# Optimization experiments

Hardware: AMD Instinct MI355X
Metric: run time of the kernel (lower is better)

## Reference

```python
import jax, jax.numpy as jnp
import numpy as np

B, T, I, H = 128, 512, 256, 512


def setup_inputs() -> dict:
    key = jax.random.key(0)
    ks = jax.random.split(key, 13)
    s_in = 1.0 / np.sqrt(I)
    s_h = 1.0 / np.sqrt(H)
    return {
        "x": jax.random.normal(ks[0], (B, T, I), jnp.float32),
        "h0": jnp.zeros((B, H), jnp.float32),
        "w_z": jax.random.normal(ks[1], (H, I), jnp.float32) * s_in,
        "w_r": jax.random.normal(ks[2], (H, I), jnp.float32) * s_in,
        "w_h": jax.random.normal(ks[3], (H, I), jnp.float32) * s_in,
        "r_z": jax.random.normal(ks[4], (H, H), jnp.float32) * s_h,
        "r_r": jax.random.normal(ks[5], (H, H), jnp.float32) * s_h,
        "r_h": jax.random.normal(ks[6], (H, H), jnp.float32) * s_h,
        "w_bz": jax.random.normal(ks[7], (H,), jnp.float32) * 0.1,
        "w_br": jax.random.normal(ks[8], (H,), jnp.float32) * 0.1,
        "w_bh": jax.random.normal(ks[9], (H,), jnp.float32) * 0.1,
        "r_bz": jax.random.normal(ks[10], (H,), jnp.float32) * 0.1,
        "r_br": jax.random.normal(ks[11], (H,), jnp.float32) * 0.1,
        "r_bh": jax.random.normal(ks[12], (H,), jnp.float32) * 0.1,
    }


def reference(x, h0, w_z, w_r, w_h, r_z, r_r, r_h,
              w_bz, w_br, w_bh, r_bz, r_br, r_bh):
    # ONNX GRU, linear_before_reset=0, no clip, activations = (sigmoid, tanh).
    # Precompute input-side projections across the whole sequence (same math
    # as per-step matmuls, done once as big GEMMs). Shapes: [B,T,H].
    xz = jnp.einsum('bti,hi->bth', x, w_z) + (w_bz + r_bz)
    xr = jnp.einsum('bti,hi->bth', x, w_r) + (w_br + r_br)
    xh = jnp.einsum('bti,hi->bth', x, w_h) + (w_bh + r_bh)

    # scan over time: carry h [B,H]
    def step(h, xs):
        xz_t, xr_t, xh_t = xs
        z = jax.nn.sigmoid(xz_t + h @ r_z.T)
        r = jax.nn.sigmoid(xr_t + h @ r_r.T)
        hh = jnp.tanh(xh_t + (r * h) @ r_h.T)
        h_new = (1.0 - z) * hh + z * h
        return h_new, h_new

    xs = (jnp.swapaxes(xz, 0, 1), jnp.swapaxes(xr, 0, 1), jnp.swapaxes(xh, 0, 1))
    h_last, seq = jax.lax.scan(step, h0, xs)
    outputs = jnp.swapaxes(seq, 0, 1)  # [B,T,H]
    return outputs, h_last
```

## Files before the change

kernel.cpp:

```cpp
#include <hip/hip_runtime.h>


typedef __attribute__((ext_vector_type(8))) short bf16x8;
typedef __attribute__((ext_vector_type(4))) float f32x4;
typedef unsigned short u16;
typedef unsigned int u32;
typedef unsigned long long u64;

#define B_ 128
#define T_ 512
#define I_ 256
#define H_ 512

__device__ __forceinline__ u16 f2b(float f) {
  union { float f; u32 i; } v; v.f = f;
  u32 u = v.i;
  return (u16)((u + 0x7FFFu + ((u >> 16) & 1u)) >> 16);
}

__device__ __forceinline__ u64 aload(u64* p) {
  return __hip_atomic_load(p, __ATOMIC_RELAXED, __HIP_MEMORY_SCOPE_AGENT);
}
__device__ __forceinline__ void astore(u64* p, u64 v) {
  __hip_atomic_store(p, v, __ATOMIC_RELAXED, __HIP_MEMORY_SCOPE_AGENT);
}

__device__ __forceinline__ void pollwave(u32* f, u32 tgt, int lane) {
  u32 v;
  do {
    v = (lane < 32) ? __hip_atomic_load(&f[lane], __ATOMIC_RELAXED, __HIP_MEMORY_SCOPE_AGENT)
                    : tgt;
  } while (__ballot(v >= tgt) != ~0ull);
  __builtin_amdgcn_s_waitcnt(0);
}

__device__ __forceinline__ void flag_set(u32* p, u32 v) {
  __builtin_amdgcn_s_waitcnt(0);
  __hip_atomic_store(p, v, __ATOMIC_RELAXED, __HIP_MEMORY_SCOPE_AGENT);
}

__global__ void prep_weights(const float* __restrict__ rz, const float* __restrict__ rr,
                             const float* __restrict__ rh, const float* __restrict__ wz,
                             const float* __restrict__ wr, const float* __restrict__ wh,
                             u16* __restrict__ wout) {
  int idx = blockIdx.x * 256 + threadIdx.x;
  if (idx >= 1179648) return;
  float v;
  if (idx < 262144)       v = rz[idx];
  else if (idx < 524288)  v = rr[idx - 262144];
  else if (idx < 786432)  v = rh[idx - 524288];
  else if (idx < 917504)  v = wz[idx - 786432];
  else if (idx < 1048576) v = wr[idx - 917504];
  else                    v = wh[idx - 1048576];
  wout[idx] = f2b(v);
}

__global__ __launch_bounds__(256, 1) void gru_persist(
    const float* __restrict__ x, const float* __restrict__ h0,
    const u16* __restrict__ wsW,
    const float* __restrict__ bwz, const float* __restrict__ bwr, const float* __restrict__ bwh,
    const float* __restrict__ brz, const float* __restrict__ brr, const float* __restrict__ brh,
    float* __restrict__ out, u64* __restrict__ hbq, u64* __restrict__ rhbq,
    u32* __restrict__ flags)
{
  const int tid  = threadIdx.x;
  const int wv   = tid >> 6;
  const int lane = tid & 63;
  const int n    = lane & 15;
  const int q    = lane >> 4;
  const int c    = blockIdx.x >> 3;
  const int w    = blockIdx.x & 7;
  const int nj   = w * 64 + wv * 16 + n;
  const int b0   = c * 16;

  const u16* wrz = wsW;
  const u16* wrr = wsW + 262144;
  const u16* wrh = wsW + 524288;
  const u16* wwz = wsW + 786432;
  const u16* wwr = wsW + 917504;
  const u16* wwh = wsW + 1048576;

  __shared__ __align__(16) u16 sA[16 * 512];
  __shared__ __align__(16) u16 sB[16 * 512];
  __shared__ __align__(16) u16 sX[16 * 256];
  __shared__ __align__(16) u16 sT[4 * 256];

  bf16x8 rzf[16], rrf[16], rhf[16], wzf[8], wrf[8], whf[8];
#pragma unroll
  for (int kb = 0; kb < 16; ++kb) {
    rzf[kb] = *(const bf16x8*)&wrz[nj * H_ + kb * 32 + q * 8];
    rrf[kb] = *(const bf16x8*)&wrr[nj * H_ + kb * 32 + q * 8];
    rhf[kb] = *(const bf16x8*)&wrh[nj * H_ + kb * 32 + q * 8];
  }
#pragma unroll
  for (int kb = 0; kb < 8; ++kb) {
    wzf[kb] = *(const bf16x8*)&wwz[nj * I_ + kb * 32 + q * 8];
    wrf[kb] = *(const bf16x8*)&wwr[nj * I_ + kb * 32 + q * 8];
    whf[kb] = *(const bf16x8*)&wwh[nj * I_ + kb * 32 + q * 8];
  }

  const float bz  = bwz[nj] + brz[nj];
  const float brg = bwr[nj] + brr[nj];
  const float bhg = bwh[nj] + brh[nj];

  float hold[4];
#pragma unroll
  for (int i = 0; i < 4; ++i) hold[i] = h0[(b0 + q * 4 + i) * H_ + nj];

  u32* hf = flags + c * 64;
  u32* rf = flags + c * 64 + 32;
  const int myflag = w * 4 + wv;

  const int prow = lane >> 2, pcq = lane & 3;
  const int pubidx = ((b0 + prow) * H_ + w * 64 + wv * 16 + pcq * 4) >> 2;
  u16* sTw = &sT[wv * 256];

  {
#pragma unroll
    for (int i = 0; i < 4; ++i) sTw[(q * 4 + i) * 16 + n] = f2b(hold[i]);
    __threadfence_block();
    astore(&hbq[pubidx], *(const u64*)&sTw[prow * 16 + pcq * 4]);
    if (lane == 0) flag_set(&hf[myflag], 1u);
    else __builtin_amdgcn_s_waitcnt(0);
  }

  for (int t = 0; t < T_; ++t) {
    __syncthreads();

#pragma unroll
    for (int it = 0; it < 2; ++it) {
      int id = it * 256 + tid;
      int row = id >> 5, kc = id & 31;
      const float* src = &x[(b0 + row) * (T_ * I_) + t * I_ + kc * 8];
      float4 v0 = *(const float4*)src;
      float4 v1 = *(const float4*)(src + 4);
      union { u16 u[8]; bf16x8 v; } pk;
      pk.u[0] = f2b(v0.x); pk.u[1] = f2b(v0.y); pk.u[2] = f2b(v0.z); pk.u[3] = f2b(v0.w);
      pk.u[4] = f2b(v1.x); pk.u[5] = f2b(v1.y); pk.u[6] = f2b(v1.z); pk.u[7] = f2b(v1.w);
      *(bf16x8*)&sX[row * 256 + (kc ^ (row & 7)) * 8] = pk.v;
    }

    pollwave(hf, (u32)(t + 1), lane);
#pragma unroll
    for (int it = 0; it < 4; ++it) {
      int id = it * 256 + tid;
      int row = id >> 6, kc = id & 63;
      int base = ((b0 + row) * H_ + kc * 8) >> 2;
      union { u64 qd[2]; bf16x8 v; } u;
      u.qd[0] = aload(&hbq[base]);
      u.qd[1] = aload(&hbq[base + 1]);
      *(bf16x8*)&sA[row * 512 + (kc ^ (row & 7)) * 8] = u.v;
    }
    __syncthreads();

    f32x4 az0 = {0.f,0.f,0.f,0.f}, az1 = {0.f,0.f,0.f,0.f};
    f32x4 ar0 = {0.f,0.f,0.f,0.f}, ar1 = {0.f,0.f,0.f,0.f};
#pragma unroll
    for (int kb = 0; kb < 16; kb += 2) {
      bf16x8 a0 = *(const bf16x8*)&sA[n * 512 + ((kb * 4 + q) ^ (n & 7)) * 8];
      az0 = __builtin_amdgcn_mfma_f32_16x16x32_bf16(a0, rzf[kb], az0, 0, 0, 0);
      ar0 = __builtin_amdgcn_mfma_f32_16x16x32_bf16(a0, rrf[kb], ar0, 0, 0, 0);
      bf16x8 a1 = *(const bf16x8*)&sA[n * 512 + (((kb + 1) * 4 + q) ^ (n & 7)) * 8];
      az1 = __builtin_amdgcn_mfma_f32_16x16x32_bf16(a1, rzf[kb + 1], az1, 0, 0, 0);
      ar1 = __builtin_amdgcn_mfma_f32_16x16x32_bf16(a1, rrf[kb + 1], ar1, 0, 0, 0);
    }
#pragma unroll
    for (int kb = 0; kb < 8; kb += 2) {
      bf16x8 a0 = *(const bf16x8*)&sX[n * 256 + ((kb * 4 + q) ^ (n & 7)) * 8];
      az0 = __builtin_amdgcn_mfma_f32_16x16x32_bf16(a0, wzf[kb], az0, 0, 0, 0);
      ar0 = __builtin_amdgcn_mfma_f32_16x16x32_bf16(a0, wrf[kb], ar0, 0, 0, 0);
      bf16x8 a1 = *(const bf16x8*)&sX[n * 256 + (((kb + 1) * 4 + q) ^ (n & 7)) * 8];
      az1 = __builtin_amdgcn_mfma_f32_16x16x32_bf16(a1, wzf[kb + 1], az1, 0, 0, 0);
      ar1 = __builtin_amdgcn_mfma_f32_16x16x32_bf16(a1, wrf[kb + 1], ar1, 0, 0, 0);
    }

    float zreg[4];
#pragma unroll
    for (int i = 0; i < 4; ++i) {
      zreg[i] = 1.f / (1.f + __expf(-(az0[i] + az1[i] + bz)));
      float rv = 1.f / (1.f + __expf(-(ar0[i] + ar1[i] + brg)));
      sTw[(q * 4 + i) * 16 + n] = f2b(rv * hold[i]);
    }
    __threadfence_block();
    astore(&rhbq[pubidx], *(const u64*)&sTw[prow * 16 + pcq * 4]);
    if (lane == 0) flag_set(&rf[myflag], (u32)(t + 1));

    f32x4 ah0 = {0.f,0.f,0.f,0.f}, ah1 = {0.f,0.f,0.f,0.f};
#pragma unroll
    for (int kb = 0; kb < 8; kb += 2) {
      bf16x8 a0 = *(const bf16x8*)&sX[n * 256 + ((kb * 4 + q) ^ (n & 7)) * 8];
      ah0 = __builtin_amdgcn_mfma_f32_16x16x32_bf16(a0, whf[kb], ah0, 0, 0, 0);
      bf16x8 a1 = *(const bf16x8*)&sX[n * 256 + (((kb + 1) * 4 + q) ^ (n & 7)) * 8];
      ah1 = __builtin_amdgcn_mfma_f32_16x16x32_bf16(a1, whf[kb + 1], ah1, 0, 0, 0);
    }

    pollwave(rf, (u32)(t + 1), lane);
#pragma unroll
    for (int it = 0; it < 4; ++it) {
      int id = it * 256 + tid;
      int row = id >> 6, kc = id & 63;
      int base = ((b0 + row) * H_ + kc * 8) >> 2;
      union { u64 qd[2]; bf16x8 v; } u;
      u.qd[0] = aload(&rhbq[base]);
      u.qd[1] = aload(&rhbq[base + 1]);
      *(bf16x8*)&sB[row * 512 + (kc ^ (row & 7)) * 8] = u.v;
    }
    __syncthreads();

#pragma unroll
    for (int kb = 0; kb < 16; kb += 2) {
      bf16x8 a0 = *(const bf16x8*)&sB[n * 512 + ((kb * 4 + q) ^ (n & 7)) * 8];
      ah0 = __builtin_amdgcn_mfma_f32_16x16x32_bf16(a0, rhf[kb], ah0, 0, 0, 0);
      bf16x8 a1 = *(const bf16x8*)&sB[n * 512 + (((kb + 1) * 4 + q) ^ (n & 7)) * 8];
      ah1 = __builtin_amdgcn_mfma_f32_16x16x32_bf16(a1, rhf[kb + 1], ah1, 0, 0, 0);
    }

#pragma unroll
    for (int i = 0; i < 4; ++i) {
      float hhv = tanhf(ah0[i] + ah1[i] + bhg);
      float hn  = (1.f - zreg[i]) * hhv + zreg[i] * hold[i];
      hold[i] = hn;
      out[(b0 + q * 4 + i) * (T_ * H_) + t * H_ + nj] = hn;
      if (t == T_ - 1) out[B_ * T_ * H_ + (b0 + q * 4 + i) * H_ + nj] = hn;
      sTw[(q * 4 + i) * 16 + n] = f2b(hn);
    }
    __threadfence_block();
    astore(&hbq[pubidx], *(const u64*)&sTw[prow * 16 + pcq * 4]);
    if (lane == 0) flag_set(&hf[myflag], (u32)(t + 2));
  }
}

extern "C" void kernel_launch(void* const* d_in, const int* in_sizes, int n_in,
                              void* d_out, int out_size, void* d_ws, size_t ws_size,
                              hipStream_t stream) {
  const float* xp   = (const float*)d_in[0];
  const float* h0p  = (const float*)d_in[1];
  const float* wzp  = (const float*)d_in[2];
  const float* wrp  = (const float*)d_in[3];
  const float* whp  = (const float*)d_in[4];
  const float* rzp  = (const float*)d_in[5];
  const float* rrp  = (const float*)d_in[6];
  const float* rhp  = (const float*)d_in[7];
  const float* bwzp = (const float*)d_in[8];
  const float* bwrp = (const float*)d_in[9];
  const float* bwhp = (const float*)d_in[10];
  const float* brzp = (const float*)d_in[11];
  const float* brrp = (const float*)d_in[12];
  const float* brhp = (const float*)d_in[13];

  unsigned char* ws = (unsigned char*)d_ws;
  u16* wsW  = (u16*)(ws);
  u64* hbq  = (u64*)(ws + 2359296);
  u64* rhbq = (u64*)(ws + 2490368);
  u32* flags = (u32*)(ws + 2621440);

  hipMemsetAsync(ws + 2621440, 0, 4096, stream);

  prep_weights<<<dim3(4608), dim3(256), 0, stream>>>(rzp, rrp, rhp, wzp, wrp, whp, wsW);

  gru_persist<<<dim3(64), dim3(256), 0, stream>>>(
      xp, h0p, wsW,
      bwzp, bwrp, bwhp, brzp, brrp, brhp,
      (float*)d_out, hbq, rhbq, flags);
}
```

Baseline: 4.102 ms.

## Replace flag-based cross-block sync with sentinel-valued double-buffered hidden state

Drops the per-step flag polling and shared-memory staging. Each of the 256 single-wave blocks now loads the recurrent state straight from global memory into registers and spins until no word equals an all-ones sentinel. The hidden and r*h buffers are double-buffered and reset to the sentinel by the consumer, which removes the separate flag store and __syncthreads. The input projection now runs before the wait so it overlaps with it, and the output stores are moved after publishing the state. The tradeoffs are a reliance on bf16 data never forming the sentinel pattern, more register pressure, and more memory traffic from 16 redundant per-block polling loads.

```diff
diff --git a/kernel.cpp b/kernel.cpp
--- a/kernel.cpp
+++ b/kernel.cpp
@@ -11,6 +11,8 @@
 #define T_ 512
 #define I_ 256
 #define H_ 512
+#define SLOT_ 16384
+#define SENT_ 0xFFFFFFFFFFFFFFFFull
 
 __device__ __forceinline__ u16 f2b(float f) {
   union { float f; u32 i; } v; v.f = f;
@@ -22,20 +24,6 @@
   return __hip_atomic_load(p, __ATOMIC_RELAXED, __HIP_MEMORY_SCOPE_AGENT);
 }
 __device__ __forceinline__ void astore(u64* p, u64 v) {
-  __hip_atomic_store(p, v, __ATOMIC_RELAXED, __HIP_MEMORY_SCOPE_AGENT);
-}
-
-__device__ __forceinline__ void pollwave(u32* f, u32 tgt, int lane) {
-  u32 v;
-  do {
-    v = (lane < 32) ? __hip_atomic_load(&f[lane], __ATOMIC_RELAXED, __HIP_MEMORY_SCOPE_AGENT)
-                    : tgt;
-  } while (__ballot(v >= tgt) != ~0ull);
-  __builtin_amdgcn_s_waitcnt(0);
-}
-
-__device__ __forceinline__ void flag_set(u32* p, u32 v) {
-  __builtin_amdgcn_s_waitcnt(0);
   __hip_atomic_store(p, v, __ATOMIC_RELAXED, __HIP_MEMORY_SCOPE_AGENT);
 }
 
@@ -55,22 +43,19 @@
   wout[idx] = f2b(v);
 }
 
-__global__ __launch_bounds__(256, 1) void gru_persist(
+__global__ __launch_bounds__(64, 1) void gru_persist(
     const float* __restrict__ x, const float* __restrict__ h0,
     const u16* __restrict__ wsW,
     const float* __restrict__ bwz, const float* __restrict__ bwr, const float* __restrict__ bwh,
     const float* __restrict__ brz, const float* __restrict__ brr, const float* __restrict__ brh,
-    float* __restrict__ out, u64* __restrict__ hbq, u64* __restrict__ rhbq,
-    u32* __restrict__ flags)
+    float* __restrict__ out, u64* __restrict__ hb, u64* __restrict__ rhb)
 {
-  const int tid  = threadIdx.x;
-  const int wv   = tid >> 6;
-  const int lane = tid & 63;
+  const int lane = threadIdx.x;
   const int n    = lane & 15;
   const int q    = lane >> 4;
-  const int c    = blockIdx.x >> 3;
-  const int w    = blockIdx.x & 7;
-  const int nj   = w * 64 + wv * 16 + n;
+  const int c    = blockIdx.x >> 5;
+  const int sl   = blockIdx.x & 31;
+  const int nj   = sl * 16 + n;
   const int b0   = c * 16;
 
   const u16* wrz = wsW;
@@ -80,11 +65,6 @@
   const u16* wwr = wsW + 917504;
   const u16* wwh = wsW + 1048576;
 
-  __shared__ __align__(16) u16 sA[16 * 512];
-  __shared__ __align__(16) u16 sB[16 * 512];
-  __shared__ __align__(16) u16 sX[16 * 256];
-  __shared__ __align__(16) u16 sT[4 * 256];
-
   bf16x8 rzf[16], rrf[16], rhf[16], wzf[8], wrf[8], whf[8];
 #pragma unroll
   for (int kb = 0; kb < 16; ++kb) {
@@ -107,71 +87,79 @@
 #pragma unroll
   for (int i = 0; i < 4; ++i) hold[i] = h0[(b0 + q * 4 + i) * H_ + nj];
 
-  u32* hf = flags + c * 64;
-  u32* rf = flags + c * 64 + 32;
-  const int myflag = w * 4 + wv;
+  __shared__ __align__(8) u16 sT[256];
 
   const int prow = lane >> 2, pcq = lane & 3;
-  const int pubidx = ((b0 + prow) * H_ + w * 64 + wv * 16 + pcq * 4) >> 2;
-  u16* sTw = &sT[wv * 256];
-
-  {
-#pragma unroll
-    for (int i = 0; i < 4; ++i) sTw[(q * 4 + i) * 16 + n] = f2b(hold[i]);
-    __threadfence_block();
-    astore(&hbq[pubidx], *(const u64*)&sTw[prow * 16 + pcq * 4]);
-    if (lane == 0) flag_set(&hf[myflag], 1u);
-    else __builtin_amdgcn_s_waitcnt(0);
-  }
+  const int pubidx = ((b0 + prow) * H_ + sl * 16 + pcq * 4) >> 2;
+  const int gb = ((b0 + n) * H_) >> 2;
+
+#pragma unroll
+  for (int i = 0; i < 4; ++i) sT[(q * 4 + i) * 16 + n] = f2b(hold[i]);
+  __threadfence_block();
+  astore(&hb[pubidx], *(const u64*)&sT[prow * 16 + pcq * 4]);
 
   for (int t = 0; t < T_; ++t) {
-    __syncthreads();
-
-#pragma unroll
-    for (int it = 0; it < 2; ++it) {
-      int id = it * 256 + tid;
-      int row = id >> 5, kc = id & 31;
-      const float* src = &x[(b0 + row) * (T_ * I_) + t * I_ + kc * 8];
-      float4 v0 = *(const float4*)src;
-      float4 v1 = *(const float4*)(src + 4);
+    const int so = (t & 1) * SLOT_;
+    const int sn = SLOT_ - so;
+    u64* hbC = hb + so;
+    u64* hbN = hb + sn;
+    u64* rhC = rhb + so;
+    u64* rhP = rhb + sn;
+
+    u64 w0[16], w1[16];
+#pragma unroll
+    for (int kb = 0; kb < 16; ++kb) {
+      w0[kb] = aload(&hbC[gb + kb * 8 + q * 2]);
+      w1[kb] = aload(&hbC[gb + kb * 8 + q * 2 + 1]);
+    }
+
+    bf16x8 xf[8];
+    const float* xrow = &x[(b0 + n) * (T_ * I_) + t * I_ + q * 8];
+#pragma unroll
+    for (int kb = 0; kb < 8; ++kb) {
+      float4 v0 = *(const float4*)(xrow + kb * 32);
+      float4 v1 = *(const float4*)(xrow + kb * 32 + 4);
       union { u16 u[8]; bf16x8 v; } pk;
       pk.u[0] = f2b(v0.x); pk.u[1] = f2b(v0.y); pk.u[2] = f2b(v0.z); pk.u[3] = f2b(v0.w);
       pk.u[4] = f2b(v1.x); pk.u[5] = f2b(v1.y); pk.u[6] = f2b(v1.z); pk.u[7] = f2b(v1.w);
-      *(bf16x8*)&sX[row * 256 + (kc ^ (row & 7)) * 8] = pk.v;
-    }
-
-    pollwave(hf, (u32)(t + 1), lane);
-#pragma unroll
-    for (int it = 0; it < 4; ++it) {
-      int id = it * 256 + tid;
-      int row = id >> 6, kc = id & 63;
-      int base = ((b0 + row) * H_ + kc * 8) >> 2;
-      union { u64 qd[2]; bf16x8 v; } u;
-      u.qd[0] = aload(&hbq[base]);
-      u.qd[1] = aload(&hbq[base + 1]);
-      *(bf16x8*)&sA[row * 512 + (kc ^ (row & 7)) * 8] = u.v;
-    }
-    __syncthreads();
-
-    f32x4 az0 = {0.f,0.f,0.f,0.f}, az1 = {0.f,0.f,0.f,0.f};
-    f32x4 ar0 = {0.f,0.f,0.f,0.f}, ar1 = {0.f,0.f,0.f,0.f};
+      xf[kb] = pk.v;
+    }
+    f32x4 az0 = {0.f, 0.f, 0.f, 0.f};
+    f32x4 az1 = az0, ar0 = az0, ar1 = az0, ah0 = az0, ah1 = az0;
+#pragma unroll
+    for (int kb = 0; kb < 8; kb += 2) {
+      az0 = __builtin_amdgcn_mfma_f32_16x16x32_bf16(xf[kb], wzf[kb], az0, 0, 0, 0);
+      ar0 = __builtin_amdgcn_mfma_f32_16x16x32_bf16(xf[kb], wrf[kb], ar0, 0, 0, 0);
+      ah0 = __builtin_amdgcn_mfma_f32_16x16x32_bf16(xf[kb], whf[kb], ah0, 0, 0, 0);
+      az1 = __builtin_amdgcn_mfma_f32_16x16x32_bf16(xf[kb + 1], wzf[kb + 1], az1, 0, 0, 0);
+      ar1 = __builtin_amdgcn_mfma_f32_16x16x32_bf16(xf[kb + 1], wrf[kb + 1], ar1, 0, 0, 0);
+      ah1 = __builtin_amdgcn_mfma_f32_16x16x32_bf16(xf[kb + 1], whf[kb + 1], ah1, 0, 0, 0);
+    }
+
+    for (;;) {
+      bool ok = true;
+#pragma unroll
+      for (int kb = 0; kb < 16; ++kb)
+        ok = ok & (w0[kb] != SENT_) & (w1[kb] != SENT_);
+      if (__ballot(ok) == ~0ull) break;
+#pragma unroll
+      for (int kb = 0; kb < 16; ++kb) {
+        if (w0[kb] == SENT_) w0[kb] = aload(&hbC[gb + kb * 8 + q * 2]);
+        if (w1[kb] == SENT_) w1[kb] = aload(&hbC[gb + kb * 8 + q * 2 + 1]);
+      }
+    }
+
+    astore(&rhP[pubidx], SENT_);
+
 #pragma unroll
     for (int kb = 0; kb < 16; kb += 2) {
-      bf16x8 a0 = *(const bf16x8*)&sA[n * 512 + ((kb * 4 + q) ^ (n & 7)) * 8];
-      az0 = __builtin_amdgcn_mfma_f32_16x16x32_bf16(a0, rzf[kb], az0, 0, 0, 0);
-      ar0 = __builtin_amdgcn_mfma_f32_16x16x32_bf16(a0, rrf[kb], ar0, 0, 0, 0);
-      bf16x8 a1 = *(const bf16x8*)&sA[n * 512 + (((kb + 1) * 4 + q) ^ (n & 7)) * 8];
-      az1 = __builtin_amdgcn_mfma_f32_16x16x32_bf16(a1, rzf[kb + 1], az1, 0, 0, 0);
-      ar1 = __builtin_amdgcn_mfma_f32_16x16x32_bf16(a1, rrf[kb + 1], ar1, 0, 0, 0);
-    }
-#pragma unroll
-    for (int kb = 0; kb < 8; kb += 2) {
-      bf16x8 a0 = *(const bf16x8*)&sX[n * 256 + ((kb * 4 + q) ^ (n & 7)) * 8];
-      az0 = __builtin_amdgcn_mfma_f32_16x16x32_bf16(a0, wzf[kb], az0, 0, 0, 0);
-      ar0 = __builtin_amdgcn_mfma_f32_16x16x32_bf16(a0, wrf[kb], ar0, 0, 0, 0);
-      bf16x8 a1 = *(const bf16x8*)&sX[n * 256 + (((kb + 1) * 4 + q) ^ (n & 7)) * 8];
-      az1 = __builtin_amdgcn_mfma_f32_16x16x32_bf16(a1, wzf[kb + 1], az1, 0, 0, 0);
-      ar1 = __builtin_amdgcn_mfma_f32_16x16x32_bf16(a1, wrf[kb + 1], ar1, 0, 0, 0);
+      union { u64 qd[2]; bf16x8 v; } a0, a1;
+      a0.qd[0] = w0[kb];     a0.qd[1] = w1[kb];
+      a1.qd[0] = w0[kb + 1]; a1.qd[1] = w1[kb + 1];
+      az0 = __builtin_amdgcn_mfma_f32_16x16x32_bf16(a0.v, rzf[kb], az0, 0, 0, 0);
+      ar0 = __builtin_amdgcn_mfma_f32_16x16x32_bf16(a0.v, rrf[kb], ar0, 0, 0, 0);
+      az1 = __builtin_amdgcn_mfma_f32_16x16x32_bf16(a1.v, rzf[kb + 1], az1, 0, 0, 0);
+      ar1 = __builtin_amdgcn_mfma_f32_16x16x32_bf16(a1.v, rrf[kb + 1], ar1, 0, 0, 0);
     }
 
     float zreg[4];
@@ -179,40 +167,38 @@
     for (int i = 0; i < 4; ++i) {
       zreg[i] = 1.f / (1.f + __expf(-(az0[i] + az1[i] + bz)));
       float rv = 1.f / (1.f + __expf(-(ar0[i] + ar1[i] + brg)));
-      sTw[(q * 4 + i) * 16 + n] = f2b(rv * hold[i]);
+      sT[(q * 4 + i) * 16 + n] = f2b(rv * hold[i]);
     }
     __threadfence_block();
-    astore(&rhbq[pubidx], *(const u64*)&sTw[prow * 16 + pcq * 4]);
-    if (lane == 0) flag_set(&rf[myflag], (u32)(t + 1));
-
-    f32x4 ah0 = {0.f,0.f,0.f,0.f}, ah1 = {0.f,0.f,0.f,0.f};
-#pragma unroll
-    for (int kb = 0; kb < 8; kb += 2) {
-      bf16x8 a0 = *(const bf16x8*)&sX[n * 256 + ((kb * 4 + q) ^ (n & 7)) * 8];
-      ah0 = __builtin_amdgcn_mfma_f32_16x16x32_bf16(a0, whf[kb], ah0, 0, 0, 0);
-      bf16x8 a1 = *(const bf16x8*)&sX[n * 256 + (((kb + 1) * 4 + q) ^ (n & 7)) * 8];
-      ah1 = __builtin_amdgcn_mfma_f32_16x16x32_bf16(a1, whf[kb + 1], ah1, 0, 0, 0);
-    }
-
-    pollwave(rf, (u32)(t + 1), lane);
-#pragma unroll
-    for (int it = 0; it < 4; ++it) {
-      int id = it * 256 + tid;
-      int row = id >> 6, kc = id & 63;
-      int base = ((b0 + row) * H_ + kc * 8) >> 2;
-      union { u64 qd[2]; bf16x8 v; } u;
-      u.qd[0] = aload(&rhbq[base]);
-      u.qd[1] = aload(&rhbq[base + 1]);
-      *(bf16x8*)&sB[row * 512 + (kc ^ (row & 7)) * 8] = u.v;
-    }
-    __syncthreads();
+    astore(&rhC[pubidx], *(const u64*)&sT[prow * 16 + pcq * 4]);
+
+#pragma unroll
+    for (int kb = 0; kb < 16; ++kb) {
+      w0[kb] = aload(&rhC[gb + kb * 8 + q * 2]);
+      w1[kb] = aload(&rhC[gb + kb * 8 + q * 2 + 1]);
+    }
+    for (;;) {
+      bool ok = true;
+#pragma unroll
+      for (int kb = 0; kb < 16; ++kb)
+        ok = ok & (w0[kb] != SENT_) & (w1[kb] != SENT_);
+      if (__ballot(ok) == ~0ull) break;
+#pragma unroll
+      for (int kb = 0; kb < 16; ++kb) {
+        if (w0[kb] == SENT_) w0[kb] = aload(&rhC[gb + kb * 8 + q * 2]);
+        if (w1[kb] == SENT_) w1[kb] = aload(&rhC[gb + kb * 8 + q * 2 + 1]);
+      }
+    }
+
+    astore(&hbC[pubidx], SENT_);
 
 #pragma unroll
     for (int kb = 0; kb < 16; kb += 2) {
-      bf16x8 a0 = *(const bf16x8*)&sB[n * 512 + ((kb * 4 + q) ^ (n & 7)) * 8];
-      ah0 = __builtin_amdgcn_mfma_f32_16x16x32_bf16(a0, rhf[kb], ah0, 0, 0, 0);
-      bf16x8 a1 = *(const bf16x8*)&sB[n * 512 + (((kb + 1) * 4 + q) ^ (n & 7)) * 8];
-      ah1 = __builtin_amdgcn_mfma_f32_16x16x32_bf16(a1, rhf[kb + 1], ah1, 0, 0, 0);
+      union { u64 qd[2]; bf16x8 v; } a0, a1;
+      a0.qd[0] = w0[kb];     a0.qd[1] = w1[kb];
+      a1.qd[0] = w0[kb + 1]; a1.qd[1] = w1[kb + 1];
+      ah0 = __builtin_amdgcn_mfma_f32_16x16x32_bf16(a0.v, rhf[kb], ah0, 0, 0, 0);
+      ah1 = __builtin_amdgcn_mfma_f32_16x16x32_bf16(a1.v, rhf[kb + 1], ah1, 0, 0, 0);
     }
 
 #pragma unroll
@@ -220,13 +206,17 @@
       float hhv = tanhf(ah0[i] + ah1[i] + bhg);
       float hn  = (1.f - zreg[i]) * hhv + zreg[i] * hold[i];
       hold[i] = hn;
-      out[(b0 + q * 4 + i) * (T_ * H_) + t * H_ + nj] = hn;
-      if (t == T_ - 1) out[B_ * T_ * H_ + (b0 + q * 4 + i) * H_ + nj] = hn;
-      sTw[(q * 4 + i) * 16 + n] = f2b(hn);
+      sT[(q * 4 + i) * 16 + n] = f2b(hn);
     }
     __threadfence_block();
-    astore(&hbq[pubidx], *(const u64*)&sTw[prow * 16 + pcq * 4]);
-    if (lane == 0) flag_set(&hf[myflag], (u32)(t + 2));
+    __builtin_amdgcn_s_waitcnt(0);
+    astore(&hbN[pubidx], *(const u64*)&sT[prow * 16 + pcq * 4]);
+
+#pragma unroll
+    for (int i = 0; i < 4; ++i) {
+      out[(b0 + q * 4 + i) * (T_ * H_) + t * H_ + nj] = hold[i];
+      if (t == T_ - 1) out[B_ * T_ * H_ + (b0 + q * 4 + i) * H_ + nj] = hold[i];
+    }
   }
 }
 
@@ -249,17 +239,16 @@
   const float* brhp = (const float*)d_in[13];
 
   unsigned char* ws = (unsigned char*)d_ws;
-  u16* wsW  = (u16*)(ws);
-  u64* hbq  = (u64*)(ws + 2359296);
-  u64* rhbq = (u64*)(ws + 2490368);
-  u32* flags = (u32*)(ws + 2621440);
-
-  hipMemsetAsync(ws + 2621440, 0, 4096, stream);
+  u16* wsW = (u16*)(ws);
+  u64* hb  = (u64*)(ws + 2359296);
+  u64* rhb = (u64*)(ws + 2621440);
+
+  hipMemsetAsync(ws + 2359296, 0xFF, 524288, stream);
 
   prep_weights<<<dim3(4608), dim3(256), 0, stream>>>(rzp, rrp, rhp, wzp, wrp, whp, wsW);
 
-  gru_persist<<<dim3(64), dim3(256), 0, stream>>>(
+  gru_persist<<<dim3(256), dim3(64), 0, stream>>>(
       xp, h0p, wsW,
       bwzp, bwrp, bwhp, brzp, brrp, brhp,
-      (float*)d_out, hbq, rhbq, flags);
-}
+      (float*)d_out, hb, rhb);
+}
```

New measurement: 4.577 ms. 1.12x slower.
